# Kernel optimization log

Hardware: AMD Instinct MI355X
Metric: run time of the kernel (lower is better)

The kernel has to match this reference:

```python
import jax, jax.numpy as jnp
import numpy as np


def _log_g(x):
    # log of g(x) = where(x>=0, x+0.5, sigmoid(x)), computed stably in log space
    return jnp.where(x >= 0.0, jnp.log(jax.nn.relu(x) + 0.5), -jax.nn.softplus(-x))


def setup_inputs() -> dict:
    key = jax.random.key(0)
    k1, k2, k3, k4 = jax.random.split(key, 4)
    B, T, D, H = 4, 8192, 512, 512
    x = jax.random.normal(k1, (B, T, D), dtype=jnp.float32)
    h_prev = jax.random.uniform(k2, (B, 1, H), dtype=jnp.float32)  # positive: log(h0) taken
    W_h = jax.random.normal(k3, (H, D), dtype=jnp.float32) * (1.0 / np.sqrt(D))
    b_h = jnp.zeros((H,), dtype=jnp.float32)
    W_z = jax.random.normal(k4, (H, D), dtype=jnp.float32) * (1.0 / np.sqrt(D))
    b_z = jnp.zeros((H,), dtype=jnp.float32)
    return {"x": x, "h_prev": h_prev, "W_h": W_h, "b_h": b_h, "W_z": W_z, "b_z": b_z}


def reference(x, h_prev, W_h, b_h, W_z, b_z):
    # parallel (seq_len > 1) minGRU forward via Heinsen log-space scan
    k = jnp.einsum('btd,hd->bth', x, W_z) + b_z           # (B,T,H) gate pre-activation
    log_z = -jax.nn.softplus(-k)                          # log sigmoid(k)
    log_coeffs = -jax.nn.softplus(k)                      # log (1 - sigmoid(k))
    log_tilde_h = _log_g(jnp.einsum('btd,hd->bth', x, W_h) + b_h)
    log_h0 = jnp.log(h_prev)                              # (B,1,H)
    log_values = jnp.concatenate([log_h0, log_z + log_tilde_h], axis=1)  # (B,T+1,H)
    # a_star = [0, cumsum(log_coeffs)]
    a_star = jnp.pad(jnp.cumsum(log_coeffs, axis=1), ((0, 0), (1, 0), (0, 0)))
    log_h = a_star + jax.lax.cumlogsumexp(log_values - a_star, axis=1)
    h = jnp.exp(log_h)[:, 1:]                             # drop h0 -> (B,T,H)
    return h
```

## Files before the change

### kernel.cpp

```cpp
#include <hip/hip_runtime.h>
#include <hip/hip_bf16.h>
#include <stdint.h>

#define B_ 4
#define T_ 8192
#define D_ 512
#define H_ 512
#define M_ (B_ * T_)
#define SEG 32
#define SPB 256
#define NSEG (M_ / SEG)

typedef __attribute__((ext_vector_type(8))) short short8;
typedef __attribute__((ext_vector_type(4))) float floatx4;
typedef __attribute__((ext_vector_type(2))) unsigned int uint2e;
typedef __attribute__((ext_vector_type(2))) float float2e;
typedef __attribute__((ext_vector_type(8))) unsigned short ushort8e;

__device__ __forceinline__ unsigned short f2bf(float f) {
    union { float f; unsigned int u; } v; v.f = f;
    unsigned int u = v.u;
    u += 0x7fffu + ((u >> 16) & 1u);
    return (unsigned short)(u >> 16);
}
__device__ __forceinline__ float bf_lo(unsigned int u) {
    union { unsigned int i; float f; } a; a.i = u << 16; return a.f;
}
__device__ __forceinline__ float bf_hi(unsigned int u) {
    union { unsigned int i; float f; } a; a.i = u & 0xffff0000u; return a.f;
}
__device__ __forceinline__ unsigned int pk_cd(float c, float d) {
    return (unsigned int)f2bf(c) | ((unsigned int)f2bf(d) << 16);
}

__global__ __launch_bounds__(256)
void conv_all(const float* __restrict__ x,
              const float* __restrict__ Wz,
              const float* __restrict__ Wh,
              unsigned short* __restrict__ xbf,
              unsigned short* __restrict__ Wf)
{
    const int X8 = M_ * D_ / 8;
    const int W8 = H_ * D_ / 8;
    int i = blockIdx.x * blockDim.x + threadIdx.x;
    const float* src; unsigned short* dst; int idx;
    if (i < X8)             { src = x;  dst = xbf;                  idx = i; }
    else if (i < X8 + W8)   { src = Wz; dst = Wf;                   idx = i - X8; }
    else if (i < X8 + 2*W8) { src = Wh; dst = Wf + (size_t)H_ * D_; idx = i - X8 - W8; }
    else return;
    float4 v0 = ((const float4*)src)[idx * 2];
    float4 v1 = ((const float4*)src)[idx * 2 + 1];
    ushort8e w;
    w[0] = f2bf(v0.x); w[1] = f2bf(v0.y); w[2] = f2bf(v0.z); w[3] = f2bf(v0.w);
    w[4] = f2bf(v1.x); w[5] = f2bf(v1.y); w[6] = f2bf(v1.z); w[7] = f2bf(v1.w);
    *(ushort8e*)&dst[idx * 8] = w;
}

#define LDSB 35840

__global__ __launch_bounds__(256, 4)
void gemm_cd(const unsigned short* __restrict__ xbf,
             const unsigned short* __restrict__ Wf,
             const float* __restrict__ bz, const float* __restrict__ bh,
             unsigned int* __restrict__ cd,
             float2* __restrict__ Sagg)
{
    __shared__ __align__(16) char smem[LDSB];
    unsigned short* lds = (unsigned short*)smem;
    unsigned int*   cdl = (unsigned int*)smem;

    const int tid  = threadIdx.x;
    const int lane = tid & 63;
    const int wave = tid >> 6;
    const int xcd  = blockIdx.x & 7;
    const int nblk = (blockIdx.x >> 3) & 7;
    const int mblk = xcd * 32 + (blockIdx.x >> 6);
    const int m0 = mblk * 128;
    const int n0 = nblk * 64;
    const int wm = (wave >> 1) * 64;
    const int wn = (wave & 1) * 32;
    const int l15  = lane & 15;
    const int quad = lane >> 4;
    const int srow = lane >> 2;
    const int sp   = lane & 3;

    #define STAGE(p, kt)                                                          \
    {                                                                             \
        const int kb = (kt) * 32;                                                 \
        unsigned short* bb = lds + (p) * 8192;                                    \
        _Pragma("unroll")                                                         \
        for (int r = 0; r < 2; ++r) {                                             \
            const int chunk = r * 4 + wave;                                       \
            const int row   = chunk * 16 + srow;                                  \
            const int kp    = sp ^ (row & 3);                                     \
            __builtin_amdgcn_global_load_lds(                                     \
                (const __attribute__((address_space(1))) unsigned int*)           \
                    (xbf + (size_t)(m0 + row) * D_ + kb + kp * 8),                \
                (__attribute__((address_space(3))) unsigned int*)(bb + chunk * 512),\
                16, 0, 0);                                                        \
        }                                                                         \
        {                                                                         \
            const int row = wave * 16 + srow;                                     \
            const int kp  = sp ^ (row & 3);                                       \
            __builtin_amdgcn_global_load_lds(                                     \
                (const __attribute__((address_space(1))) unsigned int*)           \
                    (Wf + (size_t)(n0 + row) * D_ + kb + kp * 8),                 \
                (__attribute__((address_space(3))) unsigned int*)(bb + 4096 + wave * 512),\
                16, 0, 0);                                                        \
            __builtin_amdgcn_global_load_lds(                                     \
                (const __attribute__((address_space(1))) unsigned int*)           \
                    (Wf + (size_t)(512 + n0 + row) * D_ + kb + kp * 8),           \
                (__attribute__((address_space(3))) unsigned int*)(bb + 6144 + wave * 512),\
                16, 0, 0);                                                        \
        }                                                                         \
    }

    floatx4 acc_z[4][2], acc_h[4][2];
    #pragma unroll
    for (int i = 0; i < 4; ++i)
        #pragma unroll
        for (int j = 0; j < 2; ++j) { acc_z[i][j] = (floatx4)0.0f; acc_h[i][j] = (floatx4)0.0f; }

    STAGE(0, 0);

    for (int kt = 0; kt < 16; ++kt) {
        __syncthreads();
        const int base = (kt & 1) * 8192;
        short8 af[4], zf[2], hf[2];
        #pragma unroll
        for (int i = 0; i < 4; ++i) {
            const int ra = wm + i * 16 + l15;
            af[i] = *(const short8*)&lds[base + ra * 32 + ((quad ^ (ra & 3)) * 8)];
        }
        #pragma unroll
        for (int j = 0; j < 2; ++j) {
            const int rb = wn + j * 16 + l15;
            zf[j] = *(const short8*)&lds[base + 4096 + rb * 32 + ((quad ^ (rb & 3)) * 8)];
            hf[j] = *(const short8*)&lds[base + 6144 + rb * 32 + ((quad ^ (rb & 3)) * 8)];
        }
        if (kt < 15) STAGE((kt + 1) & 1, kt + 1);
        #pragma unroll
        for (int i = 0; i < 4; ++i)
            #pragma unroll
            for (int j = 0; j < 2; ++j) {
                acc_z[i][j] = __builtin_amdgcn_mfma_f32_16x16x32_bf16(zf[j], af[i], acc_z[i][j], 0, 0, 0);
                acc_h[i][j] = __builtin_amdgcn_mfma_f32_16x16x32_bf16(hf[j], af[i], acc_h[i][j], 0, 0, 0);
            }
    }

    __syncthreads();

    #pragma unroll
    for (int j = 0; j < 2; ++j) {
        const int hlb = wn + j * 16 + quad * 4;
        const float4 bzv = *(const float4*)&bz[n0 + hlb];
        const float4 bhv = *(const float4*)&bh[n0 + hlb];
        #pragma unroll
        for (int i = 0; i < 4; ++i) {
            const int mloc = wm + i * 16 + l15;
            uint4 w;
            #pragma unroll
            for (int r = 0; r < 4; ++r) {
                float kz = acc_z[i][j][r] + ((const float*)&bzv)[r];
                float hp = acc_h[i][j][r] + ((const float*)&bhv)[r];
                float c  = __builtin_amdgcn_rcpf(1.0f + __expf(kz));
                float g  = (hp >= 0.0f) ? (hp + 0.5f)
                                        : __builtin_amdgcn_rcpf(1.0f + __expf(-hp));
                float d  = (1.0f - c) * g;
                ((unsigned int*)&w)[r] = pk_cd(c, d);
            }
            *(uint4*)&cd[(size_t)(m0 + mloc) * H_ + n0 + hlb] = w;
            *(uint4*)&cdl[mloc * 68 + hlb] = w;
        }
    }

    __syncthreads();

    {
        float C = 1.0f, Dv = 0.0f;
        const int t0 = wave * 32;
        #pragma unroll
        for (int t = 0; t < 32; ++t) {
            unsigned int u = cdl[(t0 + t) * 68 + lane];
            float c = bf_lo(u), d = bf_hi(u);
            Dv = fmaf(c, Dv, d);
            C *= c;
        }
        const int chain = (m0 >> 13) * 512 + n0 + lane;
        const int seg   = ((m0 >> 5) & 255) + wave;
        Sagg[(size_t)chain * SPB + seg] = make_float2(C, Dv);
    }
    #undef STAGE
}

__global__ __launch_bounds__(256)
void interseg(const float* __restrict__ h_prev,
              const float2* __restrict__ Sagg,
              float* __restrict__ Hseg)
{
    const int chain = blockIdx.x * 4 + (threadIdx.x >> 6);
    const int lane  = threadIdx.x & 63;
    const int b = chain >> 9;
    const int h = chain & 511;
    const float2* spp = Sagg + (size_t)chain * SPB + lane * 4;
    float4 q0 = *(const float4*)&spp[0];
    float4 q1 = *(const float4*)&spp[2];
    float C = q0.x, D = q0.y;
    D = fmaf(q0.z, D, q0.w);  C *= q0.z;
    D = fmaf(q1.x, D, q1.y);  C *= q1.x;
    D = fmaf(q1.z, D, q1.w);  C *= q1.z;
    #pragma unroll
    for (int off = 1; off < 64; off <<= 1) {
        float Cp = __shfl_up(C, off, 64);
        float Dp = __shfl_up(D, off, 64);
        if (lane >= off) { D = fmaf(C, Dp, D); C *= Cp; }
    }
    float Ce = __shfl_up(C, 1, 64);
    float De = __shfl_up(D, 1, 64);
    if (lane == 0) { Ce = 1.0f; De = 0.0f; }
    const float h0 = h_prev[chain];
    float hs = fmaf(Ce, h0, De);
    float* hb = Hseg + ((size_t)b * SPB + lane * 4) * H_ + h;
    hb[0]            = hs;
    hs = fmaf(q0.x, hs, q0.y); hb[H_]     = hs;
    hs = fmaf(q0.z, hs, q0.w); hb[2 * H_] = hs;
    hs = fmaf(q1.x, hs, q1.y); hb[3 * H_] = hs;
}

__global__ __launch_bounds__(256)
void apply_scan(const unsigned int* __restrict__ cd,
                const float* __restrict__ Hseg,
                float* __restrict__ out)
{
    const int sg = blockIdx.x;
    const int h  = threadIdx.x * 2;
    float2 hsv = *(const float2*)&Hseg[(size_t)sg * H_ + h];
    float hs0 = hsv.x, hs1 = hsv.y;
    const unsigned int* base = cd + (size_t)sg * SEG * H_ + h;
    float* ob = out + (size_t)sg * SEG * H_ + h;
    #pragma unroll
    for (int t = 0; t < SEG; ++t) {
        uint2e v = *(const uint2e*)(base + (size_t)t * H_);
        hs0 = fmaf(bf_lo(v.x), hs0, bf_hi(v.x));
        hs1 = fmaf(bf_lo(v.y), hs1, bf_hi(v.y));
        float2e o; o.x = hs0; o.y = hs1;
        __builtin_nontemporal_store(o, (float2e*)(ob + (size_t)t * H_));
    }
}

extern "C" void kernel_launch(void* const* d_in, const int* in_sizes, int n_in,
                              void* d_out, int out_size, void* d_ws, size_t ws_size,
                              hipStream_t stream)
{
    const float* x      = (const float*)d_in[0];
    const float* h_prev = (const float*)d_in[1];
    const float* W_h    = (const float*)d_in[2];
    const float* b_h    = (const float*)d_in[3];
    const float* W_z    = (const float*)d_in[4];
    const float* b_z    = (const float*)d_in[5];
    float* out = (float*)d_out;

    unsigned short* xbf = (unsigned short*)d_out;

    char* ws = (char*)d_ws;
    unsigned int* cd = (unsigned int*)ws;
    size_t cd_bytes = (size_t)M_ * H_ * 4;
    unsigned short* Wf = (unsigned short*)(ws + cd_bytes);
    size_t wf_bytes = (size_t)2 * H_ * D_ * sizeof(unsigned short);
    float2* Sagg = (float2*)(ws + cd_bytes + wf_bytes);
    float*  Hseg = (float*)((char*)Sagg + (size_t)2048 * SPB * sizeof(float2));

    {
        int total8 = M_ * D_ / 8 + 2 * (H_ * D_ / 8);
        conv_all<<<dim3((total8 + 255) / 256), dim3(256), 0, stream>>>(x, W_z, W_h, xbf, Wf);
    }
    gemm_cd<<<dim3((M_ / 128) * (H_ / 64)), dim3(256), 0, stream>>>(
        xbf, Wf, b_z, b_h, cd, Sagg);
    interseg<<<dim3(512), dim3(256), 0, stream>>>(h_prev, Sagg, Hseg);
    apply_scan<<<dim3(NSEG), dim3(256), 0, stream>>>(cd, Hseg, out);
}
```

Baseline: 194.8 us.

## Fuse all four stages into one persistent kernel with grid barriers

Merges the bf16 conversion, the GEMM plus per-segment aggregation, the inter-segment scan and the apply scan into a single persistent kernel of 512 blocks, separated by software grid barriers. The aim is to remove kernel launch gaps and tail effects between the four launches. In exchange, occupancy drops (launch bounds 3 instead of 4), the GEMM tiles are processed in a strided loop, and correctness depends on all 512 blocks being co-resident for the spin barrier. An extra memset launch is added to reset the barrier counters.

```diff
diff --git a/kernel.cpp b/kernel.cpp
--- a/kernel.cpp
+++ b/kernel.cpp
@@ -10,6 +10,7 @@
 #define SEG 32
 #define SPB 256
 #define NSEG (M_ / SEG)
+#define GRID 512
 
 typedef __attribute__((ext_vector_type(8))) short short8;
 typedef __attribute__((ext_vector_type(4))) float floatx4;
@@ -33,37 +34,33 @@
     return (unsigned int)f2bf(c) | ((unsigned int)f2bf(d) << 16);
 }
 
-__global__ __launch_bounds__(256)
-void conv_all(const float* __restrict__ x,
-              const float* __restrict__ Wz,
-              const float* __restrict__ Wh,
-              unsigned short* __restrict__ xbf,
-              unsigned short* __restrict__ Wf)
-{
-    const int X8 = M_ * D_ / 8;
-    const int W8 = H_ * D_ / 8;
-    int i = blockIdx.x * blockDim.x + threadIdx.x;
-    const float* src; unsigned short* dst; int idx;
-    if (i < X8)             { src = x;  dst = xbf;                  idx = i; }
-    else if (i < X8 + W8)   { src = Wz; dst = Wf;                   idx = i - X8; }
-    else if (i < X8 + 2*W8) { src = Wh; dst = Wf + (size_t)H_ * D_; idx = i - X8 - W8; }
-    else return;
-    float4 v0 = ((const float4*)src)[idx * 2];
-    float4 v1 = ((const float4*)src)[idx * 2 + 1];
-    ushort8e w;
-    w[0] = f2bf(v0.x); w[1] = f2bf(v0.y); w[2] = f2bf(v0.z); w[3] = f2bf(v0.w);
-    w[4] = f2bf(v1.x); w[5] = f2bf(v1.y); w[6] = f2bf(v1.z); w[7] = f2bf(v1.w);
-    *(ushort8e*)&dst[idx * 8] = w;
+__device__ __forceinline__ void grid_barrier(unsigned int* bar) {
+    __syncthreads();
+    if (threadIdx.x == 0) {
+        __threadfence();
+        unsigned int g = atomicAdd(bar + 1, 0u);
+        if (atomicAdd(bar, 1u) == (unsigned)GRID - 1u) {
+            atomicExch(bar, 0u);
+            __threadfence();
+            atomicAdd(bar + 1, 1u);
+        } else {
+            while (atomicAdd(bar + 1, 0u) == g) __builtin_amdgcn_s_sleep(8);
+            __threadfence();
+        }
+    }
+    __syncthreads();
 }
 
 #define LDSB 35840
 
-__global__ __launch_bounds__(256, 4)
-void gemm_cd(const unsigned short* __restrict__ xbf,
-             const unsigned short* __restrict__ Wf,
-             const float* __restrict__ bz, const float* __restrict__ bh,
-             unsigned int* __restrict__ cd,
-             float2* __restrict__ Sagg)
+__global__ __launch_bounds__(256, 3)
+void fused_all(const float* __restrict__ x, const float* __restrict__ h_prev,
+               const float* __restrict__ Whf, const float* __restrict__ bh,
+               const float* __restrict__ Wzf, const float* __restrict__ bz,
+               float* __restrict__ out,
+               unsigned short* __restrict__ xbf, unsigned short* __restrict__ Wf,
+               unsigned int* __restrict__ cd, float2* __restrict__ Sagg,
+               float* __restrict__ Hseg, unsigned int* __restrict__ bar)
 {
     __shared__ __align__(16) char smem[LDSB];
     unsigned short* lds = (unsigned short*)smem;
@@ -72,179 +69,197 @@
     const int tid  = threadIdx.x;
     const int lane = tid & 63;
     const int wave = tid >> 6;
-    const int xcd  = blockIdx.x & 7;
-    const int nblk = (blockIdx.x >> 3) & 7;
-    const int mblk = xcd * 32 + (blockIdx.x >> 6);
-    const int m0 = mblk * 128;
-    const int n0 = nblk * 64;
-    const int wm = (wave >> 1) * 64;
-    const int wn = (wave & 1) * 32;
     const int l15  = lane & 15;
     const int quad = lane >> 4;
     const int srow = lane >> 2;
     const int sp   = lane & 3;
 
-    #define STAGE(p, kt)                                                          \
-    {                                                                             \
-        const int kb = (kt) * 32;                                                 \
-        unsigned short* bb = lds + (p) * 8192;                                    \
-        _Pragma("unroll")                                                         \
-        for (int r = 0; r < 2; ++r) {                                             \
-            const int chunk = r * 4 + wave;                                       \
-            const int row   = chunk * 16 + srow;                                  \
-            const int kp    = sp ^ (row & 3);                                     \
-            __builtin_amdgcn_global_load_lds(                                     \
-                (const __attribute__((address_space(1))) unsigned int*)           \
-                    (xbf + (size_t)(m0 + row) * D_ + kb + kp * 8),                \
-                (__attribute__((address_space(3))) unsigned int*)(bb + chunk * 512),\
-                16, 0, 0);                                                        \
-        }                                                                         \
-        {                                                                         \
-            const int row = wave * 16 + srow;                                     \
-            const int kp  = sp ^ (row & 3);                                       \
-            __builtin_amdgcn_global_load_lds(                                     \
-                (const __attribute__((address_space(1))) unsigned int*)           \
-                    (Wf + (size_t)(n0 + row) * D_ + kb + kp * 8),                 \
-                (__attribute__((address_space(3))) unsigned int*)(bb + 4096 + wave * 512),\
-                16, 0, 0);                                                        \
-            __builtin_amdgcn_global_load_lds(                                     \
-                (const __attribute__((address_space(1))) unsigned int*)           \
-                    (Wf + (size_t)(512 + n0 + row) * D_ + kb + kp * 8),           \
-                (__attribute__((address_space(3))) unsigned int*)(bb + 6144 + wave * 512),\
-                16, 0, 0);                                                        \
-        }                                                                         \
-    }
-
-    floatx4 acc_z[4][2], acc_h[4][2];
+    {
+        const int X8 = M_ * D_ / 8;
+        const int W8 = H_ * D_ / 8;
+        const int gsz = GRID * 256;
+        for (int i = blockIdx.x * 256 + tid; i < X8 + 2 * W8; i += gsz) {
+            const float* src; unsigned short* dst; int idx;
+            if (i < X8)           { src = x;   dst = xbf;                  idx = i; }
+            else if (i < X8 + W8) { src = Wzf; dst = Wf;                   idx = i - X8; }
+            else                  { src = Whf; dst = Wf + (size_t)H_ * D_; idx = i - X8 - W8; }
+            float4 v0 = ((const float4*)src)[idx * 2];
+            float4 v1 = ((const float4*)src)[idx * 2 + 1];
+            ushort8e w;
+            w[0] = f2bf(v0.x); w[1] = f2bf(v0.y); w[2] = f2bf(v0.z); w[3] = f2bf(v0.w);
+            w[4] = f2bf(v1.x); w[5] = f2bf(v1.y); w[6] = f2bf(v1.z); w[7] = f2bf(v1.w);
+            *(ushort8e*)&dst[idx * 8] = w;
+        }
+    }
+    grid_barrier(bar);
+
+    for (int tile = blockIdx.x; tile < 2048; tile += GRID) {
+        const int xcd  = tile & 7;
+        const int nblk = (tile >> 3) & 7;
+        const int mblk = xcd * 32 + (tile >> 6);
+        const int m0 = mblk * 128;
+        const int n0 = nblk * 64;
+        const int wm = (wave >> 1) * 64;
+        const int wn = (wave & 1) * 32;
+
+        __syncthreads();
+
+        #define STAGE(p, kt)                                                          \
+        {                                                                             \
+            const int kb = (kt) * 32;                                                 \
+            unsigned short* bb = lds + (p) * 8192;                                    \
+            _Pragma("unroll")                                                         \
+            for (int r = 0; r < 2; ++r) {                                             \
+                const int chunk = r * 4 + wave;                                       \
+                const int row   = chunk * 16 + srow;                                  \
+                const int kp    = sp ^ (row & 3);                                     \
+                __builtin_amdgcn_global_load_lds(                                     \
+                    (const __attribute__((address_space(1))) unsigned int*)           \
+                        (xbf + (size_t)(m0 + row) * D_ + kb + kp * 8),                \
+                    (__attribute__((address_space(3))) unsigned int*)(bb + chunk * 512),\
+                    16, 0, 0);                                                        \
+            }                                                                         \
+            {                                                                         \
+                const int row = wave * 16 + srow;                                     \
+                const int kp  = sp ^ (row & 3);                                       \
+                __builtin_amdgcn_global_load_lds(                                     \
+                    (const __attribute__((address_space(1))) unsigned int*)           \
+                        (Wf + (size_t)(n0 + row) * D_ + kb + kp * 8),                 \
+                    (__attribute__((address_space(3))) unsigned int*)(bb + 4096 + wave * 512),\
+                    16, 0, 0);                                                        \
+                __builtin_amdgcn_global_load_lds(                                     \
+                    (const __attribute__((address_space(1))) unsigned int*)           \
+                        (Wf + (size_t)(512 + n0 + row) * D_ + kb + kp * 8),           \
+                    (__attribute__((address_space(3))) unsigned int*)(bb + 6144 + wave * 512),\
+                    16, 0, 0);                                                        \
+            }                                                                         \
+        }
+
+        floatx4 acc_z[4][2], acc_h[4][2];
+        #pragma unroll
+        for (int i = 0; i < 4; ++i)
+            #pragma unroll
+            for (int j = 0; j < 2; ++j) { acc_z[i][j] = (floatx4)0.0f; acc_h[i][j] = (floatx4)0.0f; }
+
+        STAGE(0, 0);
+
+        for (int kt = 0; kt < 16; ++kt) {
+            __syncthreads();
+            const int base = (kt & 1) * 8192;
+            short8 af[4], zf[2], hf[2];
+            #pragma unroll
+            for (int i = 0; i < 4; ++i) {
+                const int ra = wm + i * 16 + l15;
+                af[i] = *(const short8*)&lds[base + ra * 32 + ((quad ^ (ra & 3)) * 8)];
+            }
+            #pragma unroll
+            for (int j = 0; j < 2; ++j) {
+                const int rb = wn + j * 16 + l15;
+                zf[j] = *(const short8*)&lds[base + 4096 + rb * 32 + ((quad ^ (rb & 3)) * 8)];
+                hf[j] = *(const short8*)&lds[base + 6144 + rb * 32 + ((quad ^ (rb & 3)) * 8)];
+            }
+            if (kt < 15) STAGE((kt + 1) & 1, kt + 1);
+            #pragma unroll
+            for (int i = 0; i < 4; ++i)
+                #pragma unroll
+                for (int j = 0; j < 2; ++j) {
+                    acc_z[i][j] = __builtin_amdgcn_mfma_f32_16x16x32_bf16(zf[j], af[i], acc_z[i][j], 0, 0, 0);
+                    acc_h[i][j] = __builtin_amdgcn_mfma_f32_16x16x32_bf16(hf[j], af[i], acc_h[i][j], 0, 0, 0);
+                }
+        }
+
+        __syncthreads();
+
+        #pragma unroll
+        for (int j = 0; j < 2; ++j) {
+            const int hlb = wn + j * 16 + quad * 4;
+            const float4 bzv = *(const float4*)&bz[n0 + hlb];
+            const float4 bhv = *(const float4*)&bh[n0 + hlb];
+            #pragma unroll
+            for (int i = 0; i < 4; ++i) {
+                const int mloc = wm + i * 16 + l15;
+                uint4 w;
+                #pragma unroll
+                for (int r = 0; r < 4; ++r) {
+                    float kz = acc_z[i][j][r] + ((const float*)&bzv)[r];
+                    float hp = acc_h[i][j][r] + ((const float*)&bhv)[r];
+                    float c  = __builtin_amdgcn_rcpf(1.0f + __expf(kz));
+                    float g  = (hp >= 0.0f) ? (hp + 0.5f)
+                                            : __builtin_amdgcn_rcpf(1.0f + __expf(-hp));
+                    float d  = (1.0f - c) * g;
+                    ((unsigned int*)&w)[r] = pk_cd(c, d);
+                }
+                *(uint4*)&cd[(size_t)(m0 + mloc) * H_ + n0 + hlb] = w;
+                *(uint4*)&cdl[mloc * 68 + hlb] = w;
+            }
+        }
+
+        __syncthreads();
+
+        {
+            float C = 1.0f, Dv = 0.0f;
+            const int t0 = wave * 32;
+            #pragma unroll
+            for (int t = 0; t < 32; ++t) {
+                unsigned int u = cdl[(t0 + t) * 68 + lane];
+                float c = bf_lo(u), d = bf_hi(u);
+                Dv = fmaf(c, Dv, d);
+                C *= c;
+            }
+            const int chain = (m0 >> 13) * 512 + n0 + lane;
+            const int seg   = ((m0 >> 5) & 255) + wave;
+            Sagg[(size_t)chain * SPB + seg] = make_float2(C, Dv);
+        }
+        #undef STAGE
+    }
+    grid_barrier(bar);
+
+    {
+        const int chain = blockIdx.x * 4 + wave;
+        const int b = chain >> 9;
+        const int h = chain & 511;
+        const float2* spp = Sagg + (size_t)chain * SPB + lane * 4;
+        float4 q0 = *(const float4*)&spp[0];
+        float4 q1 = *(const float4*)&spp[2];
+        float C = q0.x, D = q0.y;
+        D = fmaf(q0.z, D, q0.w);  C *= q0.z;
+        D = fmaf(q1.x, D, q1.y);  C *= q1.x;
+        D = fmaf(q1.z, D, q1.w);  C *= q1.z;
+        #pragma unroll
+        for (int off = 1; off < 64; off <<= 1) {
+            float Cp = __shfl_up(C, off, 64);
+            float Dp = __shfl_up(D, off, 64);
+            if (lane >= off) { D = fmaf(C, Dp, D); C *= Cp; }
+        }
+        float Ce = __shfl_up(C, 1, 64);
+        float De = __shfl_up(D, 1, 64);
+        if (lane == 0) { Ce = 1.0f; De = 0.0f; }
+        const float h0 = h_prev[chain];
+        float hs = fmaf(Ce, h0, De);
+        float* hb = Hseg + ((size_t)b * SPB + lane * 4) * H_ + h;
+        hb[0]            = hs;
+        hs = fmaf(q0.x, hs, q0.y); hb[H_]     = hs;
+        hs = fmaf(q0.z, hs, q0.w); hb[2 * H_] = hs;
+        hs = fmaf(q1.x, hs, q1.y); hb[3 * H_] = hs;
+    }
+    grid_barrier(bar);
+
     #pragma unroll
-    for (int i = 0; i < 4; ++i)
-        #pragma unroll
-        for (int j = 0; j < 2; ++j) { acc_z[i][j] = (floatx4)0.0f; acc_h[i][j] = (floatx4)0.0f; }
-
-    STAGE(0, 0);
-
-    for (int kt = 0; kt < 16; ++kt) {
-        __syncthreads();
-        const int base = (kt & 1) * 8192;
-        short8 af[4], zf[2], hf[2];
-        #pragma unroll
-        for (int i = 0; i < 4; ++i) {
-            const int ra = wm + i * 16 + l15;
-            af[i] = *(const short8*)&lds[base + ra * 32 + ((quad ^ (ra & 3)) * 8)];
-        }
-        #pragma unroll
-        for (int j = 0; j < 2; ++j) {
-            const int rb = wn + j * 16 + l15;
-            zf[j] = *(const short8*)&lds[base + 4096 + rb * 32 + ((quad ^ (rb & 3)) * 8)];
-            hf[j] = *(const short8*)&lds[base + 6144 + rb * 32 + ((quad ^ (rb & 3)) * 8)];
-        }
-        if (kt < 15) STAGE((kt + 1) & 1, kt + 1);
-        #pragma unroll
-        for (int i = 0; i < 4; ++i)
-            #pragma unroll
-            for (int j = 0; j < 2; ++j) {
-                acc_z[i][j] = __builtin_amdgcn_mfma_f32_16x16x32_bf16(zf[j], af[i], acc_z[i][j], 0, 0, 0);
-                acc_h[i][j] = __builtin_amdgcn_mfma_f32_16x16x32_bf16(hf[j], af[i], acc_h[i][j], 0, 0, 0);
-            }
-    }
-
-    __syncthreads();
-
-    #pragma unroll
-    for (int j = 0; j < 2; ++j) {
-        const int hlb = wn + j * 16 + quad * 4;
-        const float4 bzv = *(const float4*)&bz[n0 + hlb];
-        const float4 bhv = *(const float4*)&bh[n0 + hlb];
-        #pragma unroll
-        for (int i = 0; i < 4; ++i) {
-            const int mloc = wm + i * 16 + l15;
-            uint4 w;
-            #pragma unroll
-            for (int r = 0; r < 4; ++r) {
-                float kz = acc_z[i][j][r] + ((const float*)&bzv)[r];
-                float hp = acc_h[i][j][r] + ((const float*)&bhv)[r];
-                float c  = __builtin_amdgcn_rcpf(1.0f + __expf(kz));
-                float g  = (hp >= 0.0f) ? (hp + 0.5f)
-                                        : __builtin_amdgcn_rcpf(1.0f + __expf(-hp));
-                float d  = (1.0f - c) * g;
-                ((unsigned int*)&w)[r] = pk_cd(c, d);
-            }
-            *(uint4*)&cd[(size_t)(m0 + mloc) * H_ + n0 + hlb] = w;
-            *(uint4*)&cdl[mloc * 68 + hlb] = w;
-        }
-    }
-
-    __syncthreads();
-
-    {
-        float C = 1.0f, Dv = 0.0f;
-        const int t0 = wave * 32;
-        #pragma unroll
-        for (int t = 0; t < 32; ++t) {
-            unsigned int u = cdl[(t0 + t) * 68 + lane];
-            float c = bf_lo(u), d = bf_hi(u);
-            Dv = fmaf(c, Dv, d);
-            C *= c;
-        }
-        const int chain = (m0 >> 13) * 512 + n0 + lane;
-        const int seg   = ((m0 >> 5) & 255) + wave;
-        Sagg[(size_t)chain * SPB + seg] = make_float2(C, Dv);
-    }
-    #undef STAGE
-}
-
-__global__ __launch_bounds__(256)
-void interseg(const float* __restrict__ h_prev,
-              const float2* __restrict__ Sagg,
-              float* __restrict__ Hseg)
-{
-    const int chain = blockIdx.x * 4 + (threadIdx.x >> 6);
-    const int lane  = threadIdx.x & 63;
-    const int b = chain >> 9;
-    const int h = chain & 511;
-    const float2* spp = Sagg + (size_t)chain * SPB + lane * 4;
-    float4 q0 = *(const float4*)&spp[0];
-    float4 q1 = *(const float4*)&spp[2];
-    float C = q0.x, D = q0.y;
-    D = fmaf(q0.z, D, q0.w);  C *= q0.z;
-    D = fmaf(q1.x, D, q1.y);  C *= q1.x;
-    D = fmaf(q1.z, D, q1.w);  C *= q1.z;
-    #pragma unroll
-    for (int off = 1; off < 64; off <<= 1) {
-        float Cp = __shfl_up(C, off, 64);
-        float Dp = __shfl_up(D, off, 64);
-        if (lane >= off) { D = fmaf(C, Dp, D); C *= Cp; }
-    }
-    float Ce = __shfl_up(C, 1, 64);
-    float De = __shfl_up(D, 1, 64);
-    if (lane == 0) { Ce = 1.0f; De = 0.0f; }
-    const float h0 = h_prev[chain];
-    float hs = fmaf(Ce, h0, De);
-    float* hb = Hseg + ((size_t)b * SPB + lane * 4) * H_ + h;
-    hb[0]            = hs;
-    hs = fmaf(q0.x, hs, q0.y); hb[H_]     = hs;
-    hs = fmaf(q0.z, hs, q0.w); hb[2 * H_] = hs;
-    hs = fmaf(q1.x, hs, q1.y); hb[3 * H_] = hs;
-}
-
-__global__ __launch_bounds__(256)
-void apply_scan(const unsigned int* __restrict__ cd,
-                const float* __restrict__ Hseg,
-                float* __restrict__ out)
-{
-    const int sg = blockIdx.x;
-    const int h  = threadIdx.x * 2;
-    float2 hsv = *(const float2*)&Hseg[(size_t)sg * H_ + h];
-    float hs0 = hsv.x, hs1 = hsv.y;
-    const unsigned int* base = cd + (size_t)sg * SEG * H_ + h;
-    float* ob = out + (size_t)sg * SEG * H_ + h;
-    #pragma unroll
-    for (int t = 0; t < SEG; ++t) {
-        uint2e v = *(const uint2e*)(base + (size_t)t * H_);
-        hs0 = fmaf(bf_lo(v.x), hs0, bf_hi(v.x));
-        hs1 = fmaf(bf_lo(v.y), hs1, bf_hi(v.y));
-        float2e o; o.x = hs0; o.y = hs1;
-        __builtin_nontemporal_store(o, (float2e*)(ob + (size_t)t * H_));
+    for (int rep = 0; rep < 2; ++rep) {
+        const int sg = blockIdx.x + rep * GRID;
+        const int h  = tid * 2;
+        float2 hsv = *(const float2*)&Hseg[(size_t)sg * H_ + h];
+        float hs0 = hsv.x, hs1 = hsv.y;
+        const unsigned int* base = cd + (size_t)sg * SEG * H_ + h;
+        float* ob = out + (size_t)sg * SEG * H_ + h;
+        #pragma unroll
+        for (int t = 0; t < SEG; ++t) {
+            uint2e v = *(const uint2e*)(base + (size_t)t * H_);
+            hs0 = fmaf(bf_lo(v.x), hs0, bf_hi(v.x));
+            hs1 = fmaf(bf_lo(v.y), hs1, bf_hi(v.y));
+            float2e o; o.x = hs0; o.y = hs1;
+            __builtin_nontemporal_store(o, (float2e*)(ob + (size_t)t * H_));
+        }
     }
 }
 
@@ -268,14 +283,13 @@
     unsigned short* Wf = (unsigned short*)(ws + cd_bytes);
     size_t wf_bytes = (size_t)2 * H_ * D_ * sizeof(unsigned short);
     float2* Sagg = (float2*)(ws + cd_bytes + wf_bytes);
-    float*  Hseg = (float*)((char*)Sagg + (size_t)2048 * SPB * sizeof(float2));
-
-    {
-        int total8 = M_ * D_ / 8 + 2 * (H_ * D_ / 8);
-        conv_all<<<dim3((total8 + 255) / 256), dim3(256), 0, stream>>>(x, W_z, W_h, xbf, Wf);
-    }
-    gemm_cd<<<dim3((M_ / 128) * (H_ / 64)), dim3(256), 0, stream>>>(
-        xbf, Wf, b_z, b_h, cd, Sagg);
-    interseg<<<dim3(512), dim3(256), 0, stream>>>(h_prev, Sagg, Hseg);
-    apply_scan<<<dim3(NSEG), dim3(256), 0, stream>>>(cd, Hseg, out);
-}
+    size_t sagg_bytes = (size_t)2048 * SPB * sizeof(float2);
+    float*  Hseg = (float*)((char*)Sagg + sagg_bytes);
+    size_t hseg_bytes = (size_t)B_ * SPB * H_ * sizeof(float);
+    unsigned int* bar = (unsigned int*)((char*)Hseg + hseg_bytes);
+
+    hipMemsetAsync(bar, 0, 256, stream);
+
+    fused_all<<<dim3(GRID), dim3(256), 0, stream>>>(
+        x, h_prev, W_h, b_h, W_z, b_z, out, xbf, Wf, cd, Sagg, Hseg, bar);
+}
```

Result: slower. 368.4 us (+89.1%).
